# Kernel optimization log

Measured on AMD Instinct MI355X. Metric: run time of the kernel, lower is better.

## Reference

```python
import jax, jax.numpy as jnp
import numpy as np
import math

B, H, S, DK, DV = 2, 16, 2048, 64, 64


def setup_inputs() -> dict:
    key = jax.random.key(0)
    k1, k2, k3 = jax.random.split(key, 3)
    Q = jax.random.normal(k1, (B, H, S, DK), dtype=jnp.float32)
    K = jax.random.normal(k2, (B, H, S, DK), dtype=jnp.float32)
    V = jax.random.normal(k3, (B, H, S, DV), dtype=jnp.float32)
    # causal mask as in module __init__ (1 = keep, 0 = masked -> -10000)
    mask = jnp.tril(jnp.ones((S, S), dtype=jnp.int32))
    return {"Q": Q, "K": K, "V": V, "mask": mask}


def reference(Q, K, V, mask):
    d_k = Q.shape[-1]
    # [B,H,S,S] scores, scaled
    score = jnp.einsum('bhqd,bhkd->bhqk', Q, K) / math.sqrt(d_k)
    # masked_fill(mask == 0, -10000.0)
    score = jnp.where(mask == 0, jnp.float32(-10000.0), score)
    # manual numerically-stable softmax along last dim
    e = jnp.exp(score - jnp.max(score, axis=-1, keepdims=True))
    attn = e / jnp.sum(e, axis=-1, keepdims=True)
    return jnp.einsum('bhqk,bhkd->bhqd', attn, V)
```

## Files before the change

### kernel.cpp

```cpp
#include <hip/hip_runtime.h>


#define S_LEN   2048
#define D_DIM   64
#define BH_N    32
#define Q_TILE  128
#define KV_TILE 64
#define NEG_BIG (-3.0e38f)
#define CSCALE  0.18033688011112042f

typedef float     f32x16 __attribute__((ext_vector_type(16)));
typedef _Float16  f16x8  __attribute__((ext_vector_type(8)));
typedef __fp16    fp16x2 __attribute__((ext_vector_type(2)));
typedef unsigned int   u32;
typedef unsigned short u16;

__device__ __forceinline__ u32 pkrtz2(float a, float b) {
  union { fp16x2 h; u32 u; } U;
  U.h = __builtin_amdgcn_cvt_pkrtz(a, b);
  return U.u;
}

__device__ __forceinline__ void plswap(u32& a, u32& b) {
  auto r = __builtin_amdgcn_permlane32_swap((int)a, (int)b, false, false);
  a = (u32)r[0]; b = (u32)r[1];
}

__device__ __forceinline__ f32x16 mfma16(f16x8 a, f16x8 b, f32x16 c) {
  return __builtin_amdgcn_mfma_f32_32x32x16_f16(a, b, c, 0, 0, 0);
}

__device__ __forceinline__ f16x8 lds_frag(const u16* base, int row, int colByte) {
  u32 off = (u32)(row * 128 + colByte);
  off ^= ((u32)(row & 7)) << 4;
  return *(const f16x8*)((const char*)base + off);
}

__global__ __launch_bounds__(256) void vtrans_kernel(const float* __restrict__ V,
                                                     u16* __restrict__ Vt) {
  __shared__ __align__(16) float buf[64][68];
  const int bid = blockIdx.x;
  const int bh  = bid & (BH_N - 1);
  const int kv0 = (bid >> 5) * 64;
  const int t   = threadIdx.x;
  {
    const int r = t >> 2, c0 = (t & 3) * 16;
    const float* src = V + ((size_t)bh * S_LEN + kv0 + r) * D_DIM + c0;
    float4 a0 = *(const float4*)(src + 0);
    float4 a1 = *(const float4*)(src + 4);
    float4 a2 = *(const float4*)(src + 8);
    float4 a3 = *(const float4*)(src + 12);
    *(float4*)&buf[r][c0 + 0]  = a0;
    *(float4*)&buf[r][c0 + 4]  = a1;
    *(float4*)&buf[r][c0 + 8]  = a2;
    *(float4*)&buf[r][c0 + 12] = a3;
  }
  __syncthreads();
  {
    const int dv = t >> 2, kc = (t & 3) * 16;
    u32 w[8];
    #pragma unroll
    for (int j = 0; j < 8; ++j)
      w[j] = pkrtz2(buf[kc + 2 * j][dv], buf[kc + 2 * j + 1][dv]);
    u16* dst = Vt + ((size_t)bh * D_DIM + dv) * S_LEN + kv0 + kc;
    *(uint4*)(dst + 0) = make_uint4(w[0], w[1], w[2], w[3]);
    *(uint4*)(dst + 8) = make_uint4(w[4], w[5], w[6], w[7]);
  }
}

__global__ __launch_bounds__(256, 2) void attn_kernel(const float* __restrict__ Q,
                                                      const float* __restrict__ K,
                                                      const u16* __restrict__ Vt,
                                                      float* __restrict__ Out) {
  __shared__ __align__(16) u16 KS[2][64 * 64];
  __shared__ __align__(16) u16 VS[2][64 * 64];

  const int bid = blockIdx.x;
  const int bh  = bid & 31;
  const int qt  = 15 - (bid >> 5);
  const int t   = threadIdx.x;
  const int w   = t >> 6;
  const int lo31 = t & 31;
  const int hi  = (t >> 5) & 1;
  const int qb  = qt * Q_TILE + w * 32;
  const int q   = qb + lo31;

  f16x8 qf[4];
  {
    const float* qp = Q + ((size_t)bh * S_LEN + q) * D_DIM;
    #pragma unroll
    for (int kk = 0; kk < 4; ++kk) {
      const int dd = kk * 16 + hi * 8;
      float4 a = *(const float4*)(qp + dd);
      float4 b = *(const float4*)(qp + dd + 4);
      union { u32 u[4]; f16x8 v; } U;
      U.u[0] = pkrtz2(a.x * CSCALE, a.y * CSCALE);
      U.u[1] = pkrtz2(a.z * CSCALE, a.w * CSCALE);
      U.u[2] = pkrtz2(b.x * CSCALE, b.y * CSCALE);
      U.u[3] = pkrtz2(b.z * CSCALE, b.w * CSCALE);
      qf[kk] = U.v;
    }
  }

  f32x16 o0 = {};
  f32x16 o1 = {};
  float m_run = NEG_BIG;
  float r_sum = 0.0f;

  const int sr  = t >> 2;
  const int sc4 = (t & 3) * 16;
  float4 ka0, ka1, ka2, ka3;
  uint4  va0, va1;

  auto issue = [&](int kb) {
    const float* kg = K + ((size_t)bh * S_LEN + kb + sr) * D_DIM + sc4;
    ka0 = *(const float4*)(kg + 0);
    ka1 = *(const float4*)(kg + 4);
    ka2 = *(const float4*)(kg + 8);
    ka3 = *(const float4*)(kg + 12);
    const u16* vg = Vt + ((size_t)bh * D_DIM + sr) * S_LEN + kb + sc4;
    va0 = *(const uint4*)(vg + 0);
    va1 = *(const uint4*)(vg + 8);
  };
  auto commit = [&](int b) {
    const u32 base = (u32)(sr * 128 + sc4 * 2);
    const u32 sw   = ((u32)(sr & 7)) << 4;
    const u32 a0 = base ^ sw, a1 = (base + 16) ^ sw;
    uint4 k0 = make_uint4(pkrtz2(ka0.x, ka0.y), pkrtz2(ka0.z, ka0.w),
                          pkrtz2(ka1.x, ka1.y), pkrtz2(ka1.z, ka1.w));
    uint4 k1 = make_uint4(pkrtz2(ka2.x, ka2.y), pkrtz2(ka2.z, ka2.w),
                          pkrtz2(ka3.x, ka3.y), pkrtz2(ka3.z, ka3.w));
    *(uint4*)((char*)KS[b] + a0) = k0;
    *(uint4*)((char*)KS[b] + a1) = k1;
    *(uint4*)((char*)VS[b] + a0) = va0;
    *(uint4*)((char*)VS[b] + a1) = va1;
  };

  issue(0);
  commit(0);
  __syncthreads();

  const int NT = 2 * (qt + 1);
  for (int T = 0; T < NT; ++T) {
    const int cur = T & 1;
    const int kb  = T * KV_TILE;
    if (T + 1 < NT) issue((T + 1) * KV_TILE);

    if (kb <= qb) {
      const bool have1 = (kb + 32 <= qb);
      const bool dg0   = (kb == qb);
      const bool dg1   = (kb + 32 == qb);
      const u16* Kc = KS[cur];
      const u16* Vc = VS[cur];

      f32x16 s0 = {}, s1 = {};
      __builtin_amdgcn_s_setprio(1);
      #pragma unroll
      for (int kk = 0; kk < 4; ++kk) {
        f16x8 kf = lds_frag(Kc, lo31, kk * 32 + hi * 16);
        s0 = mfma16(kf, qf[kk], s0);
      }
      if (have1) {
        #pragma unroll
        for (int kk = 0; kk < 4; ++kk) {
          f16x8 kf = lds_frag(Kc, 32 + lo31, kk * 32 + hi * 16);
          s1 = mfma16(kf, qf[kk], s1);
        }
      }
      __builtin_amdgcn_s_setprio(0);

      if (dg0) {
        #pragma unroll
        for (int i = 0; i < 16; ++i) {
          const int kvloc = (i & 3) + 8 * (i >> 2) + 4 * hi;
          if (kvloc > lo31) s0[i] = NEG_BIG;
        }
      }
      if (have1 && dg1) {
        #pragma unroll
        for (int i = 0; i < 16; ++i) {
          const int kvloc = (i & 3) + 8 * (i >> 2) + 4 * hi;
          if (kvloc > lo31) s1[i] = NEG_BIG;
        }
      }

      float t8[8];
      #pragma unroll
      for (int i = 0; i < 8; ++i) t8[i] = fmaxf(s0[i], s0[i + 8]);
      if (have1) {
        #pragma unroll
        for (int i = 0; i < 8; ++i) t8[i] = fmaxf(t8[i], fmaxf(s1[i], s1[i + 8]));
      }
      float t4a = fmaxf(t8[0], t8[4]), t4b = fmaxf(t8[1], t8[5]);
      float t4c = fmaxf(t8[2], t8[6]), t4d = fmaxf(t8[3], t8[7]);
      float mt = fmaxf(fmaxf(t4a, t4b), fmaxf(t4c, t4d));
      mt = fmaxf(mt, __shfl_xor(mt, 32, 64));

      if (!__all(mt <= m_run + 8.0f)) {
        const float mn = fmaxf(m_run, mt);
        const float rs = __builtin_amdgcn_exp2f(m_run - mn);
        m_run = mn;
        r_sum *= rs;
        #pragma unroll
        for (int i = 0; i < 16; ++i) { o0[i] *= rs; o1[i] *= rs; }
      }

      float psum = 0.0f;
      u32 c0w[8], c1w[8];
      #pragma unroll
      for (int j = 0; j < 8; ++j) {
        float pa = __builtin_amdgcn_exp2f(s0[2 * j]     - m_run);
        float pb = __builtin_amdgcn_exp2f(s0[2 * j + 1] - m_run);
        psum += pa + pb;
        c0w[j] = pkrtz2(pa, pb);
      }
      if (have1) {
        #pragma unroll
        for (int j = 0; j < 8; ++j) {
          float pa = __builtin_amdgcn_exp2f(s1[2 * j]     - m_run);
          float pb = __builtin_amdgcn_exp2f(s1[2 * j + 1] - m_run);
          psum += pa + pb;
          c1w[j] = pkrtz2(pa, pb);
        }
      }
      psum += __shfl_xor(psum, 32, 64);
      r_sum += psum;

      plswap(c0w[0], c0w[2]); plswap(c0w[1], c0w[3]);
      plswap(c0w[4], c0w[6]); plswap(c0w[5], c0w[7]);
      union { u32 u[4]; f16x8 v; } B0, B1;
      B0.u[0] = c0w[0]; B0.u[1] = c0w[1]; B0.u[2] = c0w[2]; B0.u[3] = c0w[3];
      B1.u[0] = c0w[4]; B1.u[1] = c0w[5]; B1.u[2] = c0w[6]; B1.u[3] = c0w[7];

      __builtin_amdgcn_s_setprio(1);
      #pragma unroll
      for (int ks = 0; ks < 2; ++ks) {
        f16x8 va = lds_frag(Vc, lo31,      ks * 32 + hi * 16);
        f16x8 vb = lds_frag(Vc, 32 + lo31, ks * 32 + hi * 16);
        f16x8 pf = (ks == 0) ? B0.v : B1.v;
        o0 = mfma16(va, pf, o0);
        o1 = mfma16(vb, pf, o1);
      }
      __builtin_amdgcn_s_setprio(0);

      if (have1) {
        plswap(c1w[0], c1w[2]); plswap(c1w[1], c1w[3]);
        plswap(c1w[4], c1w[6]); plswap(c1w[5], c1w[7]);
        union { u32 u[4]; f16x8 v; } B2, B3;
        B2.u[0] = c1w[0]; B2.u[1] = c1w[1]; B2.u[2] = c1w[2]; B2.u[3] = c1w[3];
        B3.u[0] = c1w[4]; B3.u[1] = c1w[5]; B3.u[2] = c1w[6]; B3.u[3] = c1w[7];
        __builtin_amdgcn_s_setprio(1);
        #pragma unroll
        for (int ks = 0; ks < 2; ++ks) {
          f16x8 va = lds_frag(Vc, lo31,      64 + ks * 32 + hi * 16);
          f16x8 vb = lds_frag(Vc, 32 + lo31, 64 + ks * 32 + hi * 16);
          f16x8 pf = (ks == 0) ? B2.v : B3.v;
          o0 = mfma16(va, pf, o0);
          o1 = mfma16(vb, pf, o1);
        }
        __builtin_amdgcn_s_setprio(0);
      }
    }

    if (T + 1 < NT) commit(cur ^ 1);
    __syncthreads();
  }

  const float inv = 1.0f / r_sum;
  float* op = Out + ((size_t)bh * S_LEN + q) * D_DIM;
  #pragma unroll
  for (int g = 0; g < 4; ++g) {
    float4 s0v = make_float4(o0[4 * g + 0] * inv, o0[4 * g + 1] * inv,
                             o0[4 * g + 2] * inv, o0[4 * g + 3] * inv);
    float4 s1v = make_float4(o1[4 * g + 0] * inv, o1[4 * g + 1] * inv,
                             o1[4 * g + 2] * inv, o1[4 * g + 3] * inv);
    *(float4*)(op + g * 8 + hi * 4)      = s0v;
    *(float4*)(op + 32 + g * 8 + hi * 4) = s1v;
  }
}

extern "C" void kernel_launch(void* const* d_in, const int* in_sizes, int n_in,
                              void* d_out, int out_size, void* d_ws, size_t ws_size,
                              hipStream_t stream) {
  const float* Q = (const float*)d_in[0];
  const float* K = (const float*)d_in[1];
  const float* V = (const float*)d_in[2];
  float* Out = (float*)d_out;
  u16* Vt = (u16*)d_ws;
  vtrans_kernel<<<dim3(BH_N * (S_LEN / 64)), dim3(256), 0, stream>>>(V, Vt);
  attn_kernel<<<dim3(BH_N * (S_LEN / Q_TILE)), dim3(256), 0, stream>>>(Q, K, Vt, Out);
}
```

Measured before the change: 158.9 us.

## Split KV range across wave pairs with 64-row Q tiles and merge partial softmax

The Q tile shrinks from 128 to 64 rows, doubling the grid. Two pairs of waves now process alternating 64-wide KV blocks out of a shared 128-key staged tile, and their partial outputs, maxima and sums are merged through LDS at the end. Double buffering is replaced by a single buffer with an extra barrier, occupancy is raised to 4 blocks per CU, and the V transpose scratch layout is changed to a swizzle instead of padding. The aim is better load balance and more parallelism for the causal tail. The cost is the final reduction, more K/V reloads per query, and loss of load/compute overlap in the staging.

```diff
diff --git a/kernel.cpp b/kernel.cpp
--- a/kernel.cpp
+++ b/kernel.cpp
@@ -4,8 +4,6 @@
 #define S_LEN   2048
 #define D_DIM   64
 #define BH_N    32
-#define Q_TILE  128
-#define KV_TILE 64
 #define NEG_BIG (-3.0e38f)
 #define CSCALE  0.18033688011112042f
 
@@ -30,15 +28,20 @@
   return __builtin_amdgcn_mfma_f32_32x32x16_f16(a, b, c, 0, 0, 0);
 }
 
-__device__ __forceinline__ f16x8 lds_frag(const u16* base, int row, int colByte) {
+__device__ __forceinline__ f16x8 lds_fragK(const u16* base, int row, int colByte) {
   u32 off = (u32)(row * 128 + colByte);
   off ^= ((u32)(row & 7)) << 4;
   return *(const f16x8*)((const char*)base + off);
 }
+__device__ __forceinline__ f16x8 lds_fragV(const u16* base, int row, int colByte) {
+  u32 off = (u32)(row * 256 + colByte);
+  off ^= ((u32)(row & 15)) << 4;
+  return *(const f16x8*)((const char*)base + off);
+}
 
 __global__ __launch_bounds__(256) void vtrans_kernel(const float* __restrict__ V,
                                                      u16* __restrict__ Vt) {
-  __shared__ __align__(16) float buf[64][68];
+  __shared__ __align__(16) float buf[64 * 64];
   const int bid = blockIdx.x;
   const int bh  = bid & (BH_N - 1);
   const int kv0 = (bid >> 5) * 64;
@@ -46,48 +49,52 @@
   {
     const int r = t >> 2, c0 = (t & 3) * 16;
     const float* src = V + ((size_t)bh * S_LEN + kv0 + r) * D_DIM + c0;
-    float4 a0 = *(const float4*)(src + 0);
-    float4 a1 = *(const float4*)(src + 4);
-    float4 a2 = *(const float4*)(src + 8);
-    float4 a3 = *(const float4*)(src + 12);
-    *(float4*)&buf[r][c0 + 0]  = a0;
-    *(float4*)&buf[r][c0 + 4]  = a1;
-    *(float4*)&buf[r][c0 + 8]  = a2;
-    *(float4*)&buf[r][c0 + 12] = a3;
+    const u32 swz = ((u32)((r >> 3) & 6)) << 4;
+    #pragma unroll
+    for (int k = 0; k < 4; ++k) {
+      float4 a = *(const float4*)(src + 4 * k);
+      *(float4*)((char*)buf + (((u32)(r * 256 + (c0 + 4 * k) * 4)) ^ swz)) = a;
+    }
   }
   __syncthreads();
   {
     const int dv = t >> 2, kc = (t & 3) * 16;
     u32 w[8];
     #pragma unroll
-    for (int j = 0; j < 8; ++j)
-      w[j] = pkrtz2(buf[kc + 2 * j][dv], buf[kc + 2 * j + 1][dv]);
+    for (int j = 0; j < 8; ++j) {
+      const int r0 = kc + 2 * j, r1 = kc + 2 * j + 1;
+      float x0 = *(const float*)((char*)buf +
+                 (((u32)(r0 * 256 + dv * 4)) ^ (((u32)((r0 >> 3) & 6)) << 4)));
+      float x1 = *(const float*)((char*)buf +
+                 (((u32)(r1 * 256 + dv * 4)) ^ (((u32)((r1 >> 3) & 6)) << 4)));
+      w[j] = pkrtz2(x0, x1);
+    }
     u16* dst = Vt + ((size_t)bh * D_DIM + dv) * S_LEN + kv0 + kc;
     *(uint4*)(dst + 0) = make_uint4(w[0], w[1], w[2], w[3]);
     *(uint4*)(dst + 8) = make_uint4(w[4], w[5], w[6], w[7]);
   }
 }
 
-__global__ __launch_bounds__(256, 2) void attn_kernel(const float* __restrict__ Q,
+__global__ __launch_bounds__(256, 4) void attn_kernel(const float* __restrict__ Q,
                                                       const float* __restrict__ K,
                                                       const u16* __restrict__ Vt,
                                                       float* __restrict__ Out) {
-  __shared__ __align__(16) u16 KS[2][64 * 64];
-  __shared__ __align__(16) u16 VS[2][64 * 64];
+  __shared__ __align__(16) u16 KS[128 * 64];
+  __shared__ __align__(16) u16 VS[64 * 128];
 
   const int bid = blockIdx.x;
   const int bh  = bid & 31;
-  const int qt  = 15 - (bid >> 5);
+  const int qt  = 31 - (bid >> 5);
   const int t   = threadIdx.x;
   const int w   = t >> 6;
   const int lo31 = t & 31;
   const int hi  = (t >> 5) & 1;
-  const int qb  = qt * Q_TILE + w * 32;
-  const int q   = qb + lo31;
+  const int p   = w >> 1;
+  const int qb  = qt * 64 + (w & 1) * 32;
 
   f16x8 qf[4];
   {
-    const float* qp = Q + ((size_t)bh * S_LEN + q) * D_DIM;
+    const float* qp = Q + ((size_t)bh * S_LEN + qb + lo31) * D_DIM;
     #pragma unroll
     for (int kk = 0; kk < 4; ++kk) {
       const int dd = kk * 16 + hi * 8;
@@ -107,63 +114,65 @@
   float m_run = NEG_BIG;
   float r_sum = 0.0f;
 
-  const int sr  = t >> 2;
-  const int sc4 = (t & 3) * 16;
-  float4 ka0, ka1, ka2, ka3;
-  uint4  va0, va1;
-
-  auto issue = [&](int kb) {
-    const float* kg = K + ((size_t)bh * S_LEN + kb + sr) * D_DIM + sc4;
-    ka0 = *(const float4*)(kg + 0);
-    ka1 = *(const float4*)(kg + 4);
-    ka2 = *(const float4*)(kg + 8);
-    ka3 = *(const float4*)(kg + 12);
-    const u16* vg = Vt + ((size_t)bh * D_DIM + sr) * S_LEN + kb + sc4;
-    va0 = *(const uint4*)(vg + 0);
-    va1 = *(const uint4*)(vg + 8);
+  const int srK = t >> 1;
+  const int scK = (t & 1) * 32;
+  const int dvV = t >> 2;
+  const int kqV = (t & 3) * 32;
+  float4 kr[8];
+  uint4  vr[4];
+
+  auto issue = [&](int s) {
+    const int kb128 = s * 128;
+    const float* kg = K + ((size_t)bh * S_LEN + kb128 + srK) * D_DIM + scK;
+    #pragma unroll
+    for (int i = 0; i < 8; ++i) kr[i] = *(const float4*)(kg + 4 * i);
+    const u16* vg = Vt + ((size_t)bh * D_DIM + dvV) * S_LEN + kb128 + kqV;
+    #pragma unroll
+    for (int i = 0; i < 4; ++i) vr[i] = *(const uint4*)(vg + 8 * i);
   };
-  auto commit = [&](int b) {
-    const u32 base = (u32)(sr * 128 + sc4 * 2);
-    const u32 sw   = ((u32)(sr & 7)) << 4;
-    const u32 a0 = base ^ sw, a1 = (base + 16) ^ sw;
-    uint4 k0 = make_uint4(pkrtz2(ka0.x, ka0.y), pkrtz2(ka0.z, ka0.w),
-                          pkrtz2(ka1.x, ka1.y), pkrtz2(ka1.z, ka1.w));
-    uint4 k1 = make_uint4(pkrtz2(ka2.x, ka2.y), pkrtz2(ka2.z, ka2.w),
-                          pkrtz2(ka3.x, ka3.y), pkrtz2(ka3.z, ka3.w));
-    *(uint4*)((char*)KS[b] + a0) = k0;
-    *(uint4*)((char*)KS[b] + a1) = k1;
-    *(uint4*)((char*)VS[b] + a0) = va0;
-    *(uint4*)((char*)VS[b] + a1) = va1;
+  auto commit = [&]() {
+    const u32 kbase = (u32)(srK * 128 + scK * 2);
+    const u32 ksw   = ((u32)(srK & 7)) << 4;
+    #pragma unroll
+    for (int c = 0; c < 4; ++c) {
+      uint4 d = make_uint4(pkrtz2(kr[2*c].x, kr[2*c].y),  pkrtz2(kr[2*c].z, kr[2*c].w),
+                           pkrtz2(kr[2*c+1].x, kr[2*c+1].y), pkrtz2(kr[2*c+1].z, kr[2*c+1].w));
+      *(uint4*)((char*)KS + ((kbase + 16 * c) ^ ksw)) = d;
+    }
+    const u32 vbase = (u32)(dvV * 256 + kqV * 2);
+    const u32 vsw   = ((u32)(dvV & 15)) << 4;
+    #pragma unroll
+    for (int c = 0; c < 4; ++c)
+      *(uint4*)((char*)VS + ((vbase + 16 * c) ^ vsw)) = vr[c];
   };
 
+  const int NT = qt + 1;
+  const int NS = (NT + 1) >> 1;
+
   issue(0);
-  commit(0);
+  commit();
   __syncthreads();
 
-  const int NT = 2 * (qt + 1);
-  for (int T = 0; T < NT; ++T) {
-    const int cur = T & 1;
-    const int kb  = T * KV_TILE;
-    if (T + 1 < NT) issue((T + 1) * KV_TILE);
-
+  for (int s = 0; s < NS; ++s) {
+    if (s + 1 < NS) issue(s + 1);
+
+    const int kb = (2 * s + p) * 64;
     if (kb <= qb) {
       const bool have1 = (kb + 32 <= qb);
       const bool dg0   = (kb == qb);
       const bool dg1   = (kb + 32 == qb);
-      const u16* Kc = KS[cur];
-      const u16* Vc = VS[cur];
 
       f32x16 s0 = {}, s1 = {};
       __builtin_amdgcn_s_setprio(1);
       #pragma unroll
       for (int kk = 0; kk < 4; ++kk) {
-        f16x8 kf = lds_frag(Kc, lo31, kk * 32 + hi * 16);
+        f16x8 kf = lds_fragK(KS, p * 64 + lo31, kk * 32 + hi * 16);
         s0 = mfma16(kf, qf[kk], s0);
       }
       if (have1) {
         #pragma unroll
         for (int kk = 0; kk < 4; ++kk) {
-          f16x8 kf = lds_frag(Kc, 32 + lo31, kk * 32 + hi * 16);
+          f16x8 kf = lds_fragK(KS, p * 64 + 32 + lo31, kk * 32 + hi * 16);
           s1 = mfma16(kf, qf[kk], s1);
         }
       }
@@ -235,8 +244,8 @@
       __builtin_amdgcn_s_setprio(1);
       #pragma unroll
       for (int ks = 0; ks < 2; ++ks) {
-        f16x8 va = lds_frag(Vc, lo31,      ks * 32 + hi * 16);
-        f16x8 vb = lds_frag(Vc, 32 + lo31, ks * 32 + hi * 16);
+        f16x8 va = lds_fragV(VS, lo31,      p * 128 + ks * 32 + hi * 16);
+        f16x8 vb = lds_fragV(VS, 32 + lo31, p * 128 + ks * 32 + hi * 16);
         f16x8 pf = (ks == 0) ? B0.v : B1.v;
         o0 = mfma16(va, pf, o0);
         o1 = mfma16(vb, pf, o1);
@@ -252,8 +261,8 @@
         __builtin_amdgcn_s_setprio(1);
         #pragma unroll
         for (int ks = 0; ks < 2; ++ks) {
-          f16x8 va = lds_frag(Vc, lo31,      64 + ks * 32 + hi * 16);
-          f16x8 vb = lds_frag(Vc, 32 + lo31, 64 + ks * 32 + hi * 16);
+          f16x8 va = lds_fragV(VS, lo31,      p * 128 + 64 + ks * 32 + hi * 16);
+          f16x8 vb = lds_fragV(VS, 32 + lo31, p * 128 + 64 + ks * 32 + hi * 16);
           f16x8 pf = (ks == 0) ? B2.v : B3.v;
           o0 = mfma16(va, pf, o0);
           o1 = mfma16(vb, pf, o1);
@@ -262,20 +271,42 @@
       }
     }
 
-    if (T + 1 < NT) commit(cur ^ 1);
     __syncthreads();
-  }
-
-  const float inv = 1.0f / r_sum;
-  float* op = Out + ((size_t)bh * S_LEN + q) * D_DIM;
-  #pragma unroll
-  for (int g = 0; g < 4; ++g) {
-    float4 s0v = make_float4(o0[4 * g + 0] * inv, o0[4 * g + 1] * inv,
-                             o0[4 * g + 2] * inv, o0[4 * g + 3] * inv);
-    float4 s1v = make_float4(o1[4 * g + 0] * inv, o1[4 * g + 1] * inv,
-                             o1[4 * g + 2] * inv, o1[4 * g + 3] * inv);
-    *(float4*)(op + g * 8 + hi * 4)      = s0v;
-    *(float4*)(op + 32 + g * 8 + hi * 4) = s1v;
+    if (s + 1 < NS) { commit(); __syncthreads(); }
+  }
+
+  const int l64 = t & 63;
+  if (p == 1) {
+    float* mb = (float*)((w == 2) ? (void*)KS : (void*)VS);
+    #pragma unroll
+    for (int i = 0; i < 16; ++i) mb[i * 64 + l64] = o0[i];
+    #pragma unroll
+    for (int i = 0; i < 16; ++i) mb[(16 + i) * 64 + l64] = o1[i];
+    mb[32 * 64 + l64] = m_run;
+    mb[33 * 64 + l64] = r_sum;
+  }
+  __syncthreads();
+  if (p == 0) {
+    const float* mb = (const float*)((w == 0) ? (void*)KS : (void*)VS);
+    const float m_b = mb[32 * 64 + l64];
+    const float r_b = mb[33 * 64 + l64];
+    const float mn  = fmaxf(m_run, m_b);
+    const float sa  = __builtin_amdgcn_exp2f(m_run - mn);
+    const float sb  = __builtin_amdgcn_exp2f(m_b  - mn);
+    const float inv = 1.0f / (r_sum * sa + r_b * sb);
+    float* op = Out + ((size_t)bh * S_LEN + qb + lo31) * D_DIM;
+    #pragma unroll
+    for (int g = 0; g < 4; ++g) {
+      float4 s0v, s1v;
+      #pragma unroll
+      for (int k = 0; k < 4; ++k) {
+        const int i = 4 * g + k;
+        ((float*)&s0v)[k] = (o0[i] * sa + mb[i * 64 + l64]        * sb) * inv;
+        ((float*)&s1v)[k] = (o1[i] * sa + mb[(16 + i) * 64 + l64] * sb) * inv;
+      }
+      *(float4*)(op + g * 8 + hi * 4)      = s0v;
+      *(float4*)(op + 32 + g * 8 + hi * 4) = s1v;
+    }
   }
 }
 
@@ -288,5 +319,5 @@
   float* Out = (float*)d_out;
   u16* Vt = (u16*)d_ws;
   vtrans_kernel<<<dim3(BH_N * (S_LEN / 64)), dim3(256), 0, stream>>>(V, Vt);
-  attn_kernel<<<dim3(BH_N * (S_LEN / Q_TILE)), dim3(256), 0, stream>>>(Q, K, Vt, Out);
-}
+  attn_kernel<<<dim3(BH_N * 32), dim3(256), 0, stream>>>(Q, K, Vt, Out);
+}
```

Result: slower. 290.0 us (+82.6%).
